# Kernel tuning notes

Measured on AMD Instinct MI355X. Metric: run time of the kernel, lower is better.

Reference implementation:

```python
import jax, jax.numpy as jnp
import numpy as np

NUM_CLASSES = 1000
EMBED_DIM = 1024
BATCH = 32768
FACTOR = 0.3


def setup_inputs() -> dict:
    key = jax.random.key(0)
    k1, k2, k3 = jax.random.split(key, 3)
    embed = jax.random.normal(k1, (BATCH, EMBED_DIM), dtype=jnp.float32)
    y = jax.random.randint(k2, (BATCH,), 0, NUM_CLASSES, dtype=jnp.int64)
    centroid = jax.random.normal(k3, (NUM_CLASSES, EMBED_DIM), dtype=jnp.float32)
    return {"embed": embed, "y": y, "centroid": centroid}


def reference(embed, y, centroid):
    # Per-class sum of embeddings: equivalent to eye(C)[y].T @ embed,
    # done as a scatter-add (segment_sum) instead of a dense one-hot matmul.
    sums = jax.ops.segment_sum(embed, y, num_segments=NUM_CLASSES)  # [C, D]
    counts = jax.ops.segment_sum(
        jnp.ones((embed.shape[0],), dtype=embed.dtype), y, num_segments=NUM_CLASSES
    )  # [C] == weight.sum(dim=1)
    cur_centroid = sums / counts[:, None]  # per-class mean
    new_centroid = FACTOR * cur_centroid + (1.0 - FACTOR) * centroid
    return new_centroid
```

## Files before the change

kernel.cpp:

```cpp
#include <hip/hip_runtime.h>


#define BATCH       32768
#define EMBED_DIM   1024
#define NUM_CLASSES 1000
#define FACTOR      0.3f
#define MAXR        128
#define HALF_DIM    512

__global__ __launch_bounds__(256) void centroid_kernel(
    const float* __restrict__ embed,
    const int*   __restrict__ y,
    const float* __restrict__ centroid,
    float*       __restrict__ out)
{
    const int bid = blockIdx.x;
    const int c   = bid >> 1;
    const int h   = bid & 1;
    const int tid = threadIdx.x;
    const int d0  = h * HALF_DIM + tid * 2;

    __shared__ int rows[MAXR];
    __shared__ int nmatch;

    if (tid == 0) nmatch = 0;

    const size_t o = (size_t)c * EMBED_DIM + d0;
    const float2 cen = *reinterpret_cast<const float2*>(centroid + o);

    __syncthreads();

    #pragma unroll 8
    for (int base = 0; base < BATCH; base += 1024) {
        const int idx = base + tid * 4;
        const int4 v = *reinterpret_cast<const int4*>(y + idx);
        if (v.x == c) { int p = atomicAdd(&nmatch, 1); rows[p] = idx + 0; }
        if (v.y == c) { int p = atomicAdd(&nmatch, 1); rows[p] = idx + 1; }
        if (v.z == c) { int p = atomicAdd(&nmatch, 1); rows[p] = idx + 2; }
        if (v.w == c) { int p = atomicAdd(&nmatch, 1); rows[p] = idx + 3; }
    }
    __syncthreads();

    const int m  = nmatch;
    const int mp = (m + 15) & ~15;

    if (tid >= m && tid < mp) rows[tid] = rows[0];
    __syncthreads();

    float2 accs[4];
    #pragma unroll
    for (int a = 0; a < 4; ++a) accs[a] = make_float2(0.f, 0.f);

    for (int j = 0; j < mp; j += 16) {
        float2 v[16];
        #pragma unroll
        for (int u = 0; u < 16; ++u) {
            const int r = rows[j + u];
            v[u] = *reinterpret_cast<const float2*>(
                embed + (size_t)r * EMBED_DIM + d0);
        }
        #pragma unroll
        for (int u = 0; u < 16; ++u) {
            accs[u & 3].x += v[u].x;
            accs[u & 3].y += v[u].y;
        }
    }

    if (mp > m) {
        const float pad = (float)(mp - m);
        const int r0 = rows[0];
        const float2 v0 = *reinterpret_cast<const float2*>(
            embed + (size_t)r0 * EMBED_DIM + d0);
        accs[0].x = fmaf(-pad, v0.x, accs[0].x);
        accs[0].y = fmaf(-pad, v0.y, accs[0].y);
    }

    float2 acc;
    acc.x = (accs[0].x + accs[1].x) + (accs[2].x + accs[3].x);
    acc.y = (accs[0].y + accs[1].y) + (accs[2].y + accs[3].y);

    const float inv = 1.0f / (float)m;
    float2 res;
    res.x = FACTOR * (acc.x * inv) + (1.0f - FACTOR) * cen.x;
    res.y = FACTOR * (acc.y * inv) + (1.0f - FACTOR) * cen.y;
    *reinterpret_cast<float2*>(out + o) = res;
}

extern "C" void kernel_launch(void* const* d_in, const int* in_sizes, int n_in,
                              void* d_out, int out_size, void* d_ws, size_t ws_size,
                              hipStream_t stream) {
    const float* embed    = (const float*)d_in[0];
    const int*   y        = (const int*)d_in[1];
    const float* centroid = (const float*)d_in[2];
    float*       out      = (float*)d_out;

    centroid_kernel<<<NUM_CLASSES * 2, 256, 0, stream>>>(embed, y, centroid, out);
}
```

Before: 212.9 us.

## Pipeline label scan and embedding gather in chunks with double-buffered row lists

Measured after the change: 201.5 us (median of 2 runs). 1.06x faster.

```diff
diff --git a/kernel.cpp b/kernel.cpp
--- a/kernel.cpp
+++ b/kernel.cpp
@@ -5,8 +5,10 @@
 #define EMBED_DIM   1024
 #define NUM_CLASSES 1000
 #define FACTOR      0.3f
-#define MAXR        128
 #define HALF_DIM    512
+#define CHUNK       4096
+#define NCHUNK      (BATCH / CHUNK)
+#define MAXR        80
 
 __global__ __launch_bounds__(256) void centroid_kernel(
     const float* __restrict__ embed,
@@ -20,70 +22,80 @@
     const int tid = threadIdx.x;
     const int d0  = h * HALF_DIM + tid * 2;
 
-    __shared__ int rows[MAXR];
-    __shared__ int nmatch;
+    __shared__ int rows[2][MAXR];
+    __shared__ int nm[2];
 
-    if (tid == 0) nmatch = 0;
+    if (tid < 2) nm[tid] = 0;
 
     const size_t o = (size_t)c * EMBED_DIM + d0;
     const float2 cen = *reinterpret_cast<const float2*>(centroid + o);
 
     __syncthreads();
 
-    #pragma unroll 8
-    for (int base = 0; base < BATCH; base += 1024) {
-        const int idx = base + tid * 4;
-        const int4 v = *reinterpret_cast<const int4*>(y + idx);
-        if (v.x == c) { int p = atomicAdd(&nmatch, 1); rows[p] = idx + 0; }
-        if (v.y == c) { int p = atomicAdd(&nmatch, 1); rows[p] = idx + 1; }
-        if (v.z == c) { int p = atomicAdd(&nmatch, 1); rows[p] = idx + 2; }
-        if (v.w == c) { int p = atomicAdd(&nmatch, 1); rows[p] = idx + 3; }
+#define SCAN(ck, b)                                                         \
+    {                                                                       \
+        const int base_ = (ck) * CHUNK + tid * 4;                           \
+        _Pragma("unroll")                                                   \
+        for (int q = 0; q < 4; ++q) {                                       \
+            const int idx = base_ + q * 1024;                               \
+            const int4 v = *reinterpret_cast<const int4*>(y + idx);         \
+            if (v.x == c) { int p = atomicAdd(&nm[b], 1); rows[b][p] = idx + 0; } \
+            if (v.y == c) { int p = atomicAdd(&nm[b], 1); rows[b][p] = idx + 1; } \
+            if (v.z == c) { int p = atomicAdd(&nm[b], 1); rows[b][p] = idx + 2; } \
+            if (v.w == c) { int p = atomicAdd(&nm[b], 1); rows[b][p] = idx + 3; } \
+        }                                                                   \
     }
+
+    SCAN(0, 0)
     __syncthreads();
 
-    const int m  = nmatch;
-    const int mp = (m + 15) & ~15;
+    float2 acc0 = make_float2(0.f, 0.f);
+    float2 acc1 = make_float2(0.f, 0.f);
+    int count = 0;
 
-    if (tid >= m && tid < mp) rows[tid] = rows[0];
-    __syncthreads();
+    for (int k = 0; k < NCHUNK; ++k) {
+        const int b = k & 1;
+        const int m = nm[b];
 
-    float2 accs[4];
-    #pragma unroll
-    for (int a = 0; a < 4; ++a) accs[a] = make_float2(0.f, 0.f);
+        if (k + 1 < NCHUNK) SCAN(k + 1, b ^ 1)
 
-    for (int j = 0; j < mp; j += 16) {
-        float2 v[16];
-        #pragma unroll
-        for (int u = 0; u < 16; ++u) {
-            const int r = rows[j + u];
-            v[u] = *reinterpret_cast<const float2*>(
-                embed + (size_t)r * EMBED_DIM + d0);
+        const int mp = (m + 3) & ~3;
+        for (int j = 0; j < mp; j += 4) {
+            float2 v[4];
+            #pragma unroll
+            for (int u = 0; u < 4; ++u) {
+                const int jj = j + u;
+                const int r = rows[b][jj < m ? jj : 0];
+                v[u] = *reinterpret_cast<const float2*>(
+                    embed + (size_t)r * EMBED_DIM + d0);
+            }
+            acc0.x += v[0].x; acc0.y += v[0].y;
+            acc1.x += v[1].x; acc1.y += v[1].y;
+            acc0.x += v[2].x; acc0.y += v[2].y;
+            acc1.x += v[3].x; acc1.y += v[3].y;
         }
-        #pragma unroll
-        for (int u = 0; u < 16; ++u) {
-            accs[u & 3].x += v[u].x;
-            accs[u & 3].y += v[u].y;
+        if (mp > m) {
+            const float pad = (float)(mp - m);
+            const int r0 = rows[b][0];
+            const float2 v0 = *reinterpret_cast<const float2*>(
+                embed + (size_t)r0 * EMBED_DIM + d0);
+            acc0.x = fmaf(-pad, v0.x, acc0.x);
+            acc0.y = fmaf(-pad, v0.y, acc0.y);
         }
+        count += m;
+
+        if (tid == 0) nm[b] = 0;
+        __syncthreads();
     }
 
-    if (mp > m) {
-        const float pad = (float)(mp - m);
-        const int r0 = rows[0];
-        const float2 v0 = *reinterpret_cast<const float2*>(
-            embed + (size_t)r0 * EMBED_DIM + d0);
-        accs[0].x = fmaf(-pad, v0.x, accs[0].x);
-        accs[0].y = fmaf(-pad, v0.y, accs[0].y);
-    }
-
-    float2 acc;
-    acc.x = (accs[0].x + accs[1].x) + (accs[2].x + accs[3].x);
-    acc.y = (accs[0].y + accs[1].y) + (accs[2].y + accs[3].y);
-
-    const float inv = 1.0f / (float)m;
+    const float inv = 1.0f / (float)count;
+    const float sx = acc0.x + acc1.x;
+    const float sy = acc0.y + acc1.y;
     float2 res;
-    res.x = FACTOR * (acc.x * inv) + (1.0f - FACTOR) * cen.x;
-    res.y = FACTOR * (acc.y * inv) + (1.0f - FACTOR) * cen.y;
+    res.x = FACTOR * (sx * inv) + (1.0f - FACTOR) * cen.x;
+    res.y = FACTOR * (sy * inv) + (1.0f - FACTOR) * cen.y;
     *reinterpret_cast<float2*>(out + o) = res;
+#undef SCAN
 }
 
 extern "C" void kernel_launch(void* const* d_in, const int* in_sizes, int n_in,
```

## Pipeline label scan with embedding gather using double-buffered chunked row lists

Applied to the files above, without the earlier changes.

New measurement: 206.8 us. 1.03x faster.

```diff
diff --git a/kernel.cpp b/kernel.cpp
--- a/kernel.cpp
+++ b/kernel.cpp
@@ -5,8 +5,10 @@
 #define EMBED_DIM   1024
 #define NUM_CLASSES 1000
 #define FACTOR      0.3f
-#define MAXR        128
 #define HALF_DIM    512
+#define CHUNK       4096
+#define NCHUNK      (BATCH / CHUNK)
+#define MAXR        80
 
 __global__ __launch_bounds__(256) void centroid_kernel(
     const float* __restrict__ embed,
@@ -20,69 +22,103 @@
     const int tid = threadIdx.x;
     const int d0  = h * HALF_DIM + tid * 2;
 
-    __shared__ int rows[MAXR];
-    __shared__ int nmatch;
+    __shared__ int rows[2][MAXR];
+    __shared__ int nm[NCHUNK];
 
-    if (tid == 0) nmatch = 0;
+    if (tid < NCHUNK) nm[tid] = 0;
 
     const size_t o = (size_t)c * EMBED_DIM + d0;
     const float2 cen = *reinterpret_cast<const float2*>(centroid + o);
 
     __syncthreads();
 
-    #pragma unroll 8
-    for (int base = 0; base < BATCH; base += 1024) {
-        const int idx = base + tid * 4;
-        const int4 v = *reinterpret_cast<const int4*>(y + idx);
-        if (v.x == c) { int p = atomicAdd(&nmatch, 1); rows[p] = idx + 0; }
-        if (v.y == c) { int p = atomicAdd(&nmatch, 1); rows[p] = idx + 1; }
-        if (v.z == c) { int p = atomicAdd(&nmatch, 1); rows[p] = idx + 2; }
-        if (v.w == c) { int p = atomicAdd(&nmatch, 1); rows[p] = idx + 3; }
+    {
+        const int base_ = tid * 4;
+        #pragma unroll
+        for (int q = 0; q < 4; ++q) {
+            const int idx = base_ + q * 1024;
+            const int4 v = *reinterpret_cast<const int4*>(y + idx);
+            if (v.x == c) { int p = atomicAdd(&nm[0], 1); rows[0][p] = idx + 0; }
+            if (v.y == c) { int p = atomicAdd(&nm[0], 1); rows[0][p] = idx + 1; }
+            if (v.z == c) { int p = atomicAdd(&nm[0], 1); rows[0][p] = idx + 2; }
+            if (v.w == c) { int p = atomicAdd(&nm[0], 1); rows[0][p] = idx + 3; }
+        }
     }
-    __syncthreads();
-
-    const int m  = nmatch;
-    const int mp = (m + 15) & ~15;
-
-    if (tid >= m && tid < mp) rows[tid] = rows[0];
+    int4 yv0, yv1, yv2, yv3;
+    {
+        const int base_ = CHUNK + tid * 4;
+        yv0 = *reinterpret_cast<const int4*>(y + base_ + 0 * 1024);
+        yv1 = *reinterpret_cast<const int4*>(y + base_ + 1 * 1024);
+        yv2 = *reinterpret_cast<const int4*>(y + base_ + 2 * 1024);
+        yv3 = *reinterpret_cast<const int4*>(y + base_ + 3 * 1024);
+    }
     __syncthreads();
 
     float2 accs[4];
     #pragma unroll
     for (int a = 0; a < 4; ++a) accs[a] = make_float2(0.f, 0.f);
+    int count = 0;
 
-    for (int j = 0; j < mp; j += 16) {
-        float2 v[16];
-        #pragma unroll
-        for (int u = 0; u < 16; ++u) {
-            const int r = rows[j + u];
-            v[u] = *reinterpret_cast<const float2*>(
-                embed + (size_t)r * EMBED_DIM + d0);
+    #pragma unroll
+    for (int k = 0; k < NCHUNK; ++k) {
+        const int b = k & 1;
+        const int m = nm[k];
+        count += m;
+
+        const int mp = (m + 7) & ~7;
+        for (int j = 0; j < mp; j += 8) {
+            float2 v[8];
+            #pragma unroll
+            for (int u = 0; u < 8; ++u) {
+                const int jj = j + u;
+                const int r = rows[b][jj < m ? jj : 0];
+                v[u] = *reinterpret_cast<const float2*>(
+                    embed + (size_t)r * EMBED_DIM + d0);
+            }
+            #pragma unroll
+            for (int u = 0; u < 8; ++u) {
+                accs[u & 3].x += v[u].x;
+                accs[u & 3].y += v[u].y;
+            }
         }
-        #pragma unroll
-        for (int u = 0; u < 16; ++u) {
-            accs[u & 3].x += v[u].x;
-            accs[u & 3].y += v[u].y;
+        if (mp > m) {
+            const float pad = (float)(mp - m);
+            const int r0 = rows[b][0];
+            const float2 v0 = *reinterpret_cast<const float2*>(
+                embed + (size_t)r0 * EMBED_DIM + d0);
+            accs[0].x = fmaf(-pad, v0.x, accs[0].x);
+            accs[0].y = fmaf(-pad, v0.y, accs[0].y);
         }
+
+        if (k + 1 < NCHUNK) {
+            const int base_ = (k + 1) * CHUNK + tid * 4;
+#define CLS(yv, q)                                                          \
+            {                                                               \
+                const int i0 = base_ + (q) * 1024;                          \
+                if (yv.x == c) { int p = atomicAdd(&nm[k + 1], 1); rows[b ^ 1][p] = i0 + 0; } \
+                if (yv.y == c) { int p = atomicAdd(&nm[k + 1], 1); rows[b ^ 1][p] = i0 + 1; } \
+                if (yv.z == c) { int p = atomicAdd(&nm[k + 1], 1); rows[b ^ 1][p] = i0 + 2; } \
+                if (yv.w == c) { int p = atomicAdd(&nm[k + 1], 1); rows[b ^ 1][p] = i0 + 3; } \
+            }
+            CLS(yv0, 0) CLS(yv1, 1) CLS(yv2, 2) CLS(yv3, 3)
+#undef CLS
+        }
+        if (k + 2 < NCHUNK) {
+            const int base_ = (k + 2) * CHUNK + tid * 4;
+            yv0 = *reinterpret_cast<const int4*>(y + base_ + 0 * 1024);
+            yv1 = *reinterpret_cast<const int4*>(y + base_ + 1 * 1024);
+            yv2 = *reinterpret_cast<const int4*>(y + base_ + 2 * 1024);
+            yv3 = *reinterpret_cast<const int4*>(y + base_ + 3 * 1024);
+        }
+        __syncthreads();
     }
 
-    if (mp > m) {
-        const float pad = (float)(mp - m);
-        const int r0 = rows[0];
-        const float2 v0 = *reinterpret_cast<const float2*>(
-            embed + (size_t)r0 * EMBED_DIM + d0);
-        accs[0].x = fmaf(-pad, v0.x, accs[0].x);
-        accs[0].y = fmaf(-pad, v0.y, accs[0].y);
-    }
-
-    float2 acc;
-    acc.x = (accs[0].x + accs[1].x) + (accs[2].x + accs[3].x);
-    acc.y = (accs[0].y + accs[1].y) + (accs[2].y + accs[3].y);
-
-    const float inv = 1.0f / (float)m;
+    const float inv = 1.0f / (float)count;
+    const float sx = (accs[0].x + accs[1].x) + (accs[2].x + accs[3].x);
+    const float sy = (accs[0].y + accs[1].y) + (accs[2].y + accs[3].y);
     float2 res;
-    res.x = FACTOR * (acc.x * inv) + (1.0f - FACTOR) * cen.x;
-    res.y = FACTOR * (acc.y * inv) + (1.0f - FACTOR) * cen.y;
+    res.x = FACTOR * (sx * inv) + (1.0f - FACTOR) * cen.x;
+    res.y = FACTOR * (sy * inv) + (1.0f - FACTOR) * cen.y;
     *reinterpret_cast<float2*>(out + o) = res;
 }
 
```
